# Kernel optimization log

Hardware: AMD Instinct MI355X
Metric: run time of the kernel (lower is better)

Reference implementation:

```python
import jax, jax.numpy as jnp
import numpy as np

EMBED_DIM = 1024
N_HEADS = 16
HEAD_DIM = EMBED_DIM // N_HEADS
SEQ_LEN = 4096


def setup_inputs() -> dict:
    key = jax.random.key(0)
    k1, k2 = jax.random.split(key)
    x = jax.random.normal(k1, (SEQ_LEN, EMBED_DIM), dtype=jnp.float32)
    # Linear params (lecun-normal-ish scale)
    W_qkv = jax.random.normal(k2, (EMBED_DIM, 3 * EMBED_DIM), dtype=jnp.float32) / np.sqrt(EMBED_DIM)
    b_qkv = jnp.zeros((3 * EMBED_DIM,), dtype=jnp.float32)
    return {"x": x, "W_qkv": W_qkv, "b_qkv": b_qkv}


def reference(x, W_qkv, b_qkv):
    T = x.shape[0]
    # Fused QKV projection: [T, 3*E]
    qkv = x @ W_qkv + b_qkv
    q, k, v = jnp.split(qkv, 3, axis=-1)
    # [T, N, H]
    q = q.reshape(T, N_HEADS, HEAD_DIM)
    k = k.reshape(T, N_HEADS, HEAD_DIM)
    v = v.reshape(T, N_HEADS, HEAD_DIM)
    # Standard SDPA (module does NOT pass is_causal, so full attention)
    scale = 1.0 / np.sqrt(HEAD_DIM).astype(np.float32)
    logits = jnp.einsum("qnh,knh->nqk", q, k) * scale  # [N, T, T]
    attn = jax.nn.softmax(logits, axis=-1)
    y = jnp.einsum("nqk,knh->qnh", attn, v)  # [T, N, H]
    return y
```

## Files before the change

kernel.cpp:

```cpp
#include <hip/hip_runtime.h>

#define T_SEQ 4096
#define EMB   1024
#define NH    16
#define HD    64
#define N3    3072

#define SCL2 0.18033688011112042f

using u16 = unsigned short;
using u32 = unsigned int;
typedef __bf16 bf16x8 __attribute__((ext_vector_type(8)));
typedef float  f32x4  __attribute__((ext_vector_type(4)));
typedef float  f32x16 __attribute__((ext_vector_type(16)));
typedef u16    u16x8  __attribute__((ext_vector_type(8)));

#if __has_builtin(__builtin_amdgcn_exp2f)
#define EXP2(x) __builtin_amdgcn_exp2f(x)
#else
#define EXP2(x) exp2f(x)
#endif

__device__ inline u16 f2bf(float f) {
    union { float f; unsigned u; } v; v.f = f;
    unsigned u = v.u;
    u += 0x7FFFu + ((u >> 16) & 1u);
    return (u16)(u >> 16);
}

__global__ void convert_x_kernel(const float* __restrict__ x, u16* __restrict__ xb) {
    int i = (blockIdx.x * 256 + threadIdx.x) * 8;
    float4 a = *(const float4*)(x + i);
    float4 b = *(const float4*)(x + i + 4);
    u16x8 o;
    o[0] = f2bf(a.x); o[1] = f2bf(a.y); o[2] = f2bf(a.z); o[3] = f2bf(a.w);
    o[4] = f2bf(b.x); o[5] = f2bf(b.y); o[6] = f2bf(b.z); o[7] = f2bf(b.w);
    *(u16x8*)(xb + i) = o;
}

__global__ void transpose_w_kernel(const float* __restrict__ W, u16* __restrict__ Wt) {
    __shared__ float tile[64][72];
    int n0 = blockIdx.x * 64, k0 = blockIdx.y * 64;
    float qs = (n0 < 1024) ? SCL2 : 1.0f;
    int t = threadIdx.x;
#pragma unroll
    for (int p = 0; p < 16; ++p) {
        int idx = p * 256 + t;
        int r = idx >> 6, c = idx & 63;
        tile[r][c] = W[(k0 + r) * N3 + n0 + c];
    }
    __syncthreads();
    int c2 = t >> 2;
    int kg = (t & 3) * 16;
    u16x8 o0, o1;
#pragma unroll
    for (int j = 0; j < 8; ++j) o0[j] = f2bf(tile[kg + j][c2] * qs);
#pragma unroll
    for (int j = 0; j < 8; ++j) o1[j] = f2bf(tile[kg + 8 + j][c2] * qs);
    u16* dst = Wt + (n0 + c2) * EMB + k0 + kg;
    *(u16x8*)dst = o0;
    *(u16x8*)(dst + 8) = o1;
}

__global__ __launch_bounds__(256) void gemm_qkv_kernel(const u16* __restrict__ xb,
                                                       const u16* __restrict__ Wt,
                                                       const float* __restrict__ bias,
                                                       u16* __restrict__ qkv) {
    __shared__ __align__(16) u16 Alds[128 * 64];
    __shared__ __align__(16) u16 Blds[128 * 64];
    int tid = threadIdx.x;
    int lane = tid & 63, wave = tid >> 6;
    int wm = wave >> 1, wn = wave & 1;
    int m0 = blockIdx.y * 128, n0 = blockIdx.x * 128;
    int lr = lane & 15, lg = lane >> 4;

    f32x4 acc[4][4] = {};

    for (int kt = 0; kt < 16; ++kt) {
        int kbase = kt * 64;
#pragma unroll
        for (int p = 0; p < 4; ++p) {
            int g = p * 256 + tid;
            int row = g >> 3;
            int cg = (g & 7) << 3;
            int sg = (((cg >> 3) ^ (row & 7)) << 3);
            u16x8 va = *(const u16x8*)(xb + (m0 + row) * EMB + kbase + cg);
            *(u16x8*)&Alds[row * 64 + sg] = va;
            u16x8 vb = *(const u16x8*)(Wt + (n0 + row) * EMB + kbase + cg);
            *(u16x8*)&Blds[row * 64 + sg] = vb;
        }
        __syncthreads();
#pragma unroll
        for (int ks = 0; ks < 2; ++ks) {
            bf16x8 af[4], bf[4];
#pragma unroll
            for (int mi = 0; mi < 4; ++mi) {
                int row = wm * 64 + mi * 16 + lr;
                int sg = ((ks * 4 + lg) ^ (row & 7)) << 3;
                af[mi] = *(const bf16x8*)&Alds[row * 64 + sg];
            }
#pragma unroll
            for (int ni = 0; ni < 4; ++ni) {
                int row = wn * 64 + ni * 16 + lr;
                int sg = ((ks * 4 + lg) ^ (row & 7)) << 3;
                bf[ni] = *(const bf16x8*)&Blds[row * 64 + sg];
            }
#pragma unroll
            for (int mi = 0; mi < 4; ++mi)
#pragma unroll
                for (int ni = 0; ni < 4; ++ni)
                    acc[mi][ni] = __builtin_amdgcn_mfma_f32_16x16x32_bf16(af[mi], bf[ni], acc[mi][ni], 0, 0, 0);
        }
        __syncthreads();
    }
#pragma unroll
    for (int ni = 0; ni < 4; ++ni) {
        int n = n0 + wn * 64 + ni * 16 + lr;
        float bv = bias[n];
        if (n < 1024) bv *= SCL2;
#pragma unroll
        for (int mi = 0; mi < 4; ++mi) {
            int mrow = m0 + wm * 64 + mi * 16 + lg * 4;
#pragma unroll
            for (int r = 0; r < 4; ++r)
                qkv[(mrow + r) * N3 + n] = f2bf(acc[mi][ni][r] + bv);
        }
    }
}

__global__ void transpose_v_kernel(const u16* __restrict__ qkv, u16* __restrict__ Vt) {
    __shared__ u16 tile[64][72];
    int c0 = blockIdx.x * 64;
    int t0 = blockIdx.y * 64;
    int t = threadIdx.x;
#pragma unroll
    for (int p = 0; p < 16; ++p) {
        int idx = p * 256 + t;
        int r = idx >> 6, c = idx & 63;
        tile[r][c] = qkv[(t0 + r) * N3 + 2048 + c0 + c];
    }
    __syncthreads();
    int c2 = t >> 2;
    int kg = (t & 3) * 16;
    u16x8 o0, o1;
#pragma unroll
    for (int j = 0; j < 8; ++j) o0[j] = tile[kg + j][c2];
#pragma unroll
    for (int j = 0; j < 8; ++j) o1[j] = tile[kg + 8 + j][c2];
    u16* dst = Vt + (c0 + c2) * T_SEQ + t0 + kg;
    *(u16x8*)dst = o0;
    *(u16x8*)(dst + 8) = o1;
}

__device__ inline u32 cvtpk(float lo, float hi) {
    u32 r;
    asm("v_cvt_pk_bf16_f32 %0, %1, %2" : "=v"(r) : "v"(lo), "v"(hi));
    return r;
}

__device__ inline bf16x8 mk8(u32 w0, u32 w1, u32 w2, u32 w3) {
    union { u32 w[4]; bf16x8 v; } u;
    u.w[0] = w0; u.w[1] = w1; u.w[2] = w2; u.w[3] = w3;
    return u.v;
}

__device__ inline void pack2(f32x16 p, int hi, bf16x8& fe, bf16x8& fo) {
    u32 a0 = cvtpk(p[0], p[1]),   a1 = cvtpk(p[2], p[3]);
    u32 a2 = cvtpk(p[4], p[5]),   a3 = cvtpk(p[6], p[7]);
    u32 b0 = cvtpk(p[8], p[9]),   b1 = cvtpk(p[10], p[11]);
    u32 b2 = cvtpk(p[12], p[13]), b3 = cvtpk(p[14], p[15]);
    u32 xa0 = (u32)__shfl_xor((int)a0, 32), xa1 = (u32)__shfl_xor((int)a1, 32);
    u32 xa2 = (u32)__shfl_xor((int)a2, 32), xa3 = (u32)__shfl_xor((int)a3, 32);
    u32 xb0 = (u32)__shfl_xor((int)b0, 32), xb1 = (u32)__shfl_xor((int)b1, 32);
    u32 xb2 = (u32)__shfl_xor((int)b2, 32), xb3 = (u32)__shfl_xor((int)b3, 32);
    fe = hi ? mk8(xa2, xa3, a2, a3) : mk8(a0, a1, xa0, xa1);
    fo = hi ? mk8(xb2, xb3, b2, b3) : mk8(b0, b1, xb0, xb1);
}

#define KVROW 72

__global__ __launch_bounds__(256, 2) void attn_kernel(const u16* __restrict__ qkv,
                                                      const u16* __restrict__ Vt,
                                                      float* __restrict__ out) {
    __shared__ __align__(16) char smem[36864];
    u16* K0 = (u16*)smem;
    u16* V0 = (u16*)(smem + 9216);
    u16* K1 = (u16*)(smem + 18432);
    u16* V1 = (u16*)(smem + 27648);

    int tid = threadIdx.x, lane = tid & 63, wave = tid >> 6;
    int ql = lane & 31, hi = lane >> 5;
    int h = blockIdx.y;
    int q0 = blockIdx.x * 128;

    bf16x8 qf[4];
    {
        const u16* qp = qkv + (size_t)(q0 + wave * 32 + ql) * N3 + h * HD;
#pragma unroll
        for (int c = 0; c < 4; ++c)
            qf[c] = *(const bf16x8*)(qp + c * 16 + hi * 8);
    }

    bf16x8 ones;
    {
        union { u16x8 u; bf16x8 b; } uu;
#pragma unroll
        for (int j = 0; j < 8; ++j) uu.u[j] = 0x3F80;
        ones = uu.b;
    }

    f32x16 acc0 = {}, acc1 = {}, acc2 = {};

    int srow0 = tid >> 3, spg = tid & 7;
    int srow1 = srow0 + 32;
    const u16* kptr = qkv + EMB + h * HD;
    const u16* vptr = Vt + (size_t)(h * HD) * T_SEQ;
    int woff0 = srow0 * KVROW + spg * 8;
    int woff1 = srow1 * KVROW + spg * 8;

    u16x8 kst0 = *(const u16x8*)(kptr + (size_t)srow0 * N3 + spg * 8);
    u16x8 kst1 = *(const u16x8*)(kptr + (size_t)srow1 * N3 + spg * 8);
    u16x8 vst0 = *(const u16x8*)(vptr + (size_t)srow0 * T_SEQ + spg * 8);
    u16x8 vst1 = *(const u16x8*)(vptr + (size_t)srow1 * T_SEQ + spg * 8);

    int koff = ql * KVROW + hi * 8;

    for (int t = 0; t < 64; ++t) {
        u16* Kl = (t & 1) ? K1 : K0;
        u16* Vl = (t & 1) ? V1 : V0;
        *(u16x8*)&Kl[woff0] = kst0;
        *(u16x8*)&Kl[woff1] = kst1;
        *(u16x8*)&Vl[woff0] = vst0;
        *(u16x8*)&Vl[woff1] = vst1;
        if (t < 63) {
            const u16* kb = kptr + (size_t)(t + 1) * 64 * N3;
            const u16* vb = vptr + (t + 1) * 64;
            kst0 = *(const u16x8*)(kb + (size_t)srow0 * N3 + spg * 8);
            kst1 = *(const u16x8*)(kb + (size_t)srow1 * N3 + spg * 8);
            vst0 = *(const u16x8*)(vb + (size_t)srow0 * T_SEQ + spg * 8);
            vst1 = *(const u16x8*)(vb + (size_t)srow1 * T_SEQ + spg * 8);
        }
        __syncthreads();

        f32x16 s0 = {}, s1 = {};
#pragma unroll
        for (int c = 0; c < 4; ++c) {
            bf16x8 kf = *(const bf16x8*)&Kl[koff + c * 16];
            s0 = __builtin_amdgcn_mfma_f32_32x32x16_bf16(kf, qf[c], s0, 0, 0, 0);
        }
#pragma unroll
        for (int c = 0; c < 4; ++c) {
            bf16x8 kf = *(const bf16x8*)&Kl[koff + 32 * KVROW + c * 16];
            s1 = __builtin_amdgcn_mfma_f32_32x32x16_bf16(kf, qf[c], s1, 0, 0, 0);
        }

#pragma unroll
        for (int r = 0; r < 16; ++r) s0[r] = EXP2(s0[r]);
#pragma unroll
        for (int r = 0; r < 16; ++r) s1[r] = EXP2(s1[r]);

        bf16x8 pa0, pa1, pa2, pa3;
        pack2(s0, hi, pa0, pa1);
        pack2(s1, hi, pa2, pa3);

#pragma unroll
        for (int c = 0; c < 4; ++c) {
            bf16x8 pb = (c == 0) ? pa0 : (c == 1) ? pa1 : (c == 2) ? pa2 : pa3;
            bf16x8 vf0 = *(const bf16x8*)&Vl[koff + c * 16];
            acc0 = __builtin_amdgcn_mfma_f32_32x32x16_bf16(vf0, pb, acc0, 0, 0, 0);
            bf16x8 vf1 = *(const bf16x8*)&Vl[koff + 32 * KVROW + c * 16];
            acc1 = __builtin_amdgcn_mfma_f32_32x32x16_bf16(vf1, pb, acc1, 0, 0, 0);
            acc2 = __builtin_amdgcn_mfma_f32_32x32x16_bf16(ones, pb, acc2, 0, 0, 0);
        }
    }

    __syncthreads();

    float inv = 1.0f / acc2[0];
    float* ob = (float*)smem + wave * (32 * 68);
#pragma unroll
    for (int g = 0; g < 4; ++g) {
        f32x4 w0 = { acc0[4 * g] * inv, acc0[4 * g + 1] * inv, acc0[4 * g + 2] * inv, acc0[4 * g + 3] * inv };
        *(f32x4*)&ob[ql * 68 + 8 * g + 4 * hi] = w0;
        f32x4 w1 = { acc1[4 * g] * inv, acc1[4 * g + 1] * inv, acc1[4 * g + 2] * inv, acc1[4 * g + 3] * inv };
        *(f32x4*)&ob[ql * 68 + 32 + 8 * g + 4 * hi] = w1;
    }
    asm volatile("s_waitcnt lgkmcnt(0)" ::: "memory");
#pragma unroll
    for (int qq = 0; qq < 8; ++qq) {
        int q = qq * 4 + (lane >> 4);
        int d4 = (lane & 15) * 4;
        f32x4 v = *(const f32x4*)&ob[q * 68 + d4];
        *(f32x4*)&out[(size_t)(q0 + wave * 32 + q) * EMB + h * HD + d4] = v;
    }
}

extern "C" void kernel_launch(void* const* d_in, const int* in_sizes, int n_in,
                              void* d_out, int out_size, void* d_ws, size_t ws_size,
                              hipStream_t stream) {
    (void)in_sizes; (void)n_in; (void)out_size; (void)ws_size;
    const float* x = (const float*)d_in[0];
    const float* W = (const float*)d_in[1];
    const float* b = (const float*)d_in[2];
    float* out = (float*)d_out;

    u16* xb  = (u16*)d_ws;
    u16* Wt  = xb  + (size_t)T_SEQ * EMB;
    u16* qkv = Wt  + (size_t)N3 * EMB;
    u16* Vt  = qkv + (size_t)T_SEQ * N3;

    convert_x_kernel<<<(T_SEQ * EMB) / (256 * 8), 256, 0, stream>>>(x, xb);
    transpose_w_kernel<<<dim3(N3 / 64, EMB / 64), 256, 0, stream>>>(W, Wt);
    gemm_qkv_kernel<<<dim3(N3 / 128, T_SEQ / 128), 256, 0, stream>>>(xb, Wt, b, qkv);
    transpose_v_kernel<<<dim3(EMB / 64, T_SEQ / 64), 256, 0, stream>>>(qkv, Vt);
    attn_kernel<<<dim3(T_SEQ / 128, NH), 256, 0, stream>>>(qkv, Vt, out);
}
```

Before: 150.2 us.

## Split attention KV range across two wave groups and compute row sums on VALU

The attention block grows to 512 threads: two groups of four waves each process half of the key/value sequence for the same 128 queries, then merge their partial outputs and normalisers through shared memory. The softmax denominator is now a VALU sum of the exponentiated scores plus a cross-lane shuffle, replacing the extra MFMA against a ones vector. This aims to double the parallelism per query tile, shorten each wave's serial KV loop and drop a third of the PV-stage MFMAs. In exchange it doubles LDS per block to 72KB, which limits occupancy, and adds a reduction epilogue with extra barriers.

```diff
diff --git a/kernel.cpp b/kernel.cpp
--- a/kernel.cpp
+++ b/kernel.cpp
@@ -164,6 +164,15 @@
     return u.v;
 }
 
+__device__ inline float vsum16(f32x16 v) {
+    float a0 = v[0] + v[1],  a1 = v[2] + v[3];
+    float a2 = v[4] + v[5],  a3 = v[6] + v[7];
+    float a4 = v[8] + v[9],  a5 = v[10] + v[11];
+    float a6 = v[12] + v[13], a7 = v[14] + v[15];
+    float b0 = a0 + a1, b1 = a2 + a3, b2 = a4 + a5, b3 = a6 + a7;
+    return (b0 + b1) + (b2 + b3);
+}
+
 __device__ inline void pack2(f32x16 p, int hi, bf16x8& fe, bf16x8& fo) {
     u32 a0 = cvtpk(p[0], p[1]),   a1 = cvtpk(p[2], p[3]);
     u32 a2 = cvtpk(p[4], p[5]),   a3 = cvtpk(p[6], p[7]);
@@ -179,42 +188,40 @@
 
 #define KVROW 72
 
-__global__ __launch_bounds__(256, 2) void attn_kernel(const u16* __restrict__ qkv,
+__global__ __launch_bounds__(512, 4) void attn_kernel(const u16* __restrict__ qkv,
                                                       const u16* __restrict__ Vt,
                                                       float* __restrict__ out) {
-    __shared__ __align__(16) char smem[36864];
-    u16* K0 = (u16*)smem;
-    u16* V0 = (u16*)(smem + 9216);
-    u16* K1 = (u16*)(smem + 18432);
-    u16* V1 = (u16*)(smem + 27648);
+    __shared__ __align__(16) char smem[73728];
 
     int tid = threadIdx.x, lane = tid & 63, wave = tid >> 6;
     int ql = lane & 31, hi = lane >> 5;
+    int g = tid >> 8;
+    int wq = wave & 3;
+    int tid2 = tid & 255;
     int h = blockIdx.y;
     int q0 = blockIdx.x * 128;
 
+    char* base = smem + g * 36864;
+    u16* K0 = (u16*)base;
+    u16* V0 = (u16*)(base + 9216);
+    u16* K1 = (u16*)(base + 18432);
+    u16* V1 = (u16*)(base + 27648);
+
     bf16x8 qf[4];
     {
-        const u16* qp = qkv + (size_t)(q0 + wave * 32 + ql) * N3 + h * HD;
+        const u16* qp = qkv + (size_t)(q0 + wq * 32 + ql) * N3 + h * HD;
 #pragma unroll
         for (int c = 0; c < 4; ++c)
             qf[c] = *(const bf16x8*)(qp + c * 16 + hi * 8);
     }
 
-    bf16x8 ones;
-    {
-        union { u16x8 u; bf16x8 b; } uu;
-#pragma unroll
-        for (int j = 0; j < 8; ++j) uu.u[j] = 0x3F80;
-        ones = uu.b;
-    }
-
-    f32x16 acc0 = {}, acc1 = {}, acc2 = {};
-
-    int srow0 = tid >> 3, spg = tid & 7;
+    f32x16 acc0 = {}, acc1 = {};
+    float lrun = 0.f;
+
+    int srow0 = tid2 >> 3, spg = tid2 & 7;
     int srow1 = srow0 + 32;
-    const u16* kptr = qkv + EMB + h * HD;
-    const u16* vptr = Vt + (size_t)(h * HD) * T_SEQ;
+    const u16* kptr = qkv + (size_t)(g * 2048) * N3 + EMB + h * HD;
+    const u16* vptr = Vt + (size_t)(h * HD) * T_SEQ + g * 2048;
     int woff0 = srow0 * KVROW + spg * 8;
     int woff1 = srow1 * KVROW + spg * 8;
 
@@ -225,14 +232,14 @@
 
     int koff = ql * KVROW + hi * 8;
 
-    for (int t = 0; t < 64; ++t) {
+    for (int t = 0; t < 32; ++t) {
         u16* Kl = (t & 1) ? K1 : K0;
         u16* Vl = (t & 1) ? V1 : V0;
         *(u16x8*)&Kl[woff0] = kst0;
         *(u16x8*)&Kl[woff1] = kst1;
         *(u16x8*)&Vl[woff0] = vst0;
         *(u16x8*)&Vl[woff1] = vst1;
-        if (t < 63) {
+        if (t < 31) {
             const u16* kb = kptr + (size_t)(t + 1) * 64 * N3;
             const u16* vb = vptr + (t + 1) * 64;
             kst0 = *(const u16x8*)(kb + (size_t)srow0 * N3 + spg * 8);
@@ -259,6 +266,12 @@
 #pragma unroll
         for (int r = 0; r < 16; ++r) s1[r] = EXP2(s1[r]);
 
+        {
+            float ss = vsum16(s0) + vsum16(s1);
+            ss += __shfl_xor(ss, 32);
+            lrun += ss;
+        }
+
         bf16x8 pa0, pa1, pa2, pa3;
         pack2(s0, hi, pa0, pa1);
         pack2(s1, hi, pa2, pa3);
@@ -270,28 +283,54 @@
             acc0 = __builtin_amdgcn_mfma_f32_32x32x16_bf16(vf0, pb, acc0, 0, 0, 0);
             bf16x8 vf1 = *(const bf16x8*)&Vl[koff + 32 * KVROW + c * 16];
             acc1 = __builtin_amdgcn_mfma_f32_32x32x16_bf16(vf1, pb, acc1, 0, 0, 0);
-            acc2 = __builtin_amdgcn_mfma_f32_32x32x16_bf16(ones, pb, acc2, 0, 0, 0);
-        }
-    }
-
-    __syncthreads();
-
-    float inv = 1.0f / acc2[0];
-    float* ob = (float*)smem + wave * (32 * 68);
-#pragma unroll
-    for (int g = 0; g < 4; ++g) {
-        f32x4 w0 = { acc0[4 * g] * inv, acc0[4 * g + 1] * inv, acc0[4 * g + 2] * inv, acc0[4 * g + 3] * inv };
-        *(f32x4*)&ob[ql * 68 + 8 * g + 4 * hi] = w0;
-        f32x4 w1 = { acc1[4 * g] * inv, acc1[4 * g + 1] * inv, acc1[4 * g + 2] * inv, acc1[4 * g + 3] * inv };
-        *(f32x4*)&ob[ql * 68 + 32 + 8 * g + 4 * hi] = w1;
-    }
-    asm volatile("s_waitcnt lgkmcnt(0)" ::: "memory");
-#pragma unroll
-    for (int qq = 0; qq < 8; ++qq) {
-        int q = qq * 4 + (lane >> 4);
-        int d4 = (lane & 15) * 4;
-        f32x4 v = *(const f32x4*)&ob[q * 68 + d4];
-        *(f32x4*)&out[(size_t)(q0 + wave * 32 + q) * EMB + h * HD + d4] = v;
+        }
+    }
+
+    __syncthreads();
+
+    float* Xb = (float*)(smem + 36864);
+    float* lX = Xb + 4 * 32 * 68;
+
+    if (g == 1) {
+        float* ob = Xb + wq * (32 * 68);
+#pragma unroll
+        for (int gg = 0; gg < 4; ++gg) {
+            f32x4 w0 = { acc0[4 * gg], acc0[4 * gg + 1], acc0[4 * gg + 2], acc0[4 * gg + 3] };
+            *(f32x4*)&ob[ql * 68 + 8 * gg + 4 * hi] = w0;
+            f32x4 w1 = { acc1[4 * gg], acc1[4 * gg + 1], acc1[4 * gg + 2], acc1[4 * gg + 3] };
+            *(f32x4*)&ob[ql * 68 + 32 + 8 * gg + 4 * hi] = w1;
+        }
+        if (hi == 0) lX[wq * 32 + ql] = lrun;
+    }
+    __syncthreads();
+
+    if (g == 0) {
+        float* ob = Xb + wq * (32 * 68);
+        float inv = 1.0f / (lrun + lX[wq * 32 + ql]);
+        float* tb = (float*)smem + wq * (32 * 68);
+#pragma unroll
+        for (int gg = 0; gg < 4; ++gg) {
+            f32x4 x0 = *(const f32x4*)&ob[ql * 68 + 8 * gg + 4 * hi];
+            f32x4 w0 = { (acc0[4 * gg] + x0[0]) * inv, (acc0[4 * gg + 1] + x0[1]) * inv,
+                         (acc0[4 * gg + 2] + x0[2]) * inv, (acc0[4 * gg + 3] + x0[3]) * inv };
+            *(f32x4*)&tb[ql * 68 + 8 * gg + 4 * hi] = w0;
+            f32x4 x1 = *(const f32x4*)&ob[ql * 68 + 32 + 8 * gg + 4 * hi];
+            f32x4 w1 = { (acc1[4 * gg] + x1[0]) * inv, (acc1[4 * gg + 1] + x1[1]) * inv,
+                         (acc1[4 * gg + 2] + x1[2]) * inv, (acc1[4 * gg + 3] + x1[3]) * inv };
+            *(f32x4*)&tb[ql * 68 + 32 + 8 * gg + 4 * hi] = w1;
+        }
+    }
+    __syncthreads();
+
+    if (g == 0) {
+        float* tb = (float*)smem + wq * (32 * 68);
+#pragma unroll
+        for (int qq = 0; qq < 8; ++qq) {
+            int q = qq * 4 + (lane >> 4);
+            int d4 = (lane & 15) * 4;
+            f32x4 v = *(const f32x4*)&tb[q * 68 + d4];
+            *(f32x4*)&out[(size_t)(q0 + wq * 32 + q) * EMB + h * HD + d4] = v;
+        }
     }
 }
 
@@ -313,5 +352,5 @@
     transpose_w_kernel<<<dim3(N3 / 64, EMB / 64), 256, 0, stream>>>(W, Wt);
     gemm_qkv_kernel<<<dim3(N3 / 128, T_SEQ / 128), 256, 0, stream>>>(xb, Wt, b, qkv);
     transpose_v_kernel<<<dim3(EMB / 64, T_SEQ / 64), 256, 0, stream>>>(qkv, Vt);
-    attn_kernel<<<dim3(T_SEQ / 128, NH), 256, 0, stream>>>(qkv, Vt, out);
-}
+    attn_kernel<<<dim3(T_SEQ / 128, NH), 512, 0, stream>>>(qkv, Vt, out);
+}
```

Measured after the change: 155.9 us. 3.8% more time.

## Split attention KV range across two blocks and merge partials in combine kernel

Applied to the files above, without the earlier changes.

Attention launches a z-dimension of two, each block processing half of the keys and writing unnormalized partial outputs and row sums; a new combine kernel adds the partials and normalizes. The QKV GEMM now writes separate Q, K, V planes so K loads use a 1024 stride. Partial buffers alias dead workspace regions. This adds an extra kernel and extra global traffic for partials in exchange for more parallel blocks.

```diff
diff --git a/kernel.cpp b/kernel.cpp
--- a/kernel.cpp
+++ b/kernel.cpp
@@ -65,7 +65,7 @@
 __global__ __launch_bounds__(256) void gemm_qkv_kernel(const u16* __restrict__ xb,
                                                        const u16* __restrict__ Wt,
                                                        const float* __restrict__ bias,
-                                                       u16* __restrict__ qkv) {
+                                                       u16* __restrict__ qkv ) {
     __shared__ __align__(16) u16 Alds[128 * 64];
     __shared__ __align__(16) u16 Blds[128 * 64];
     int tid = threadIdx.x;
@@ -118,17 +118,19 @@
         int n = n0 + wn * 64 + ni * 16 + lr;
         float bv = bias[n];
         if (n < 1024) bv *= SCL2;
+        u16* pl = qkv + (size_t)(n >> 10) * ((size_t)T_SEQ * EMB);
+        int nc = n & 1023;
 #pragma unroll
         for (int mi = 0; mi < 4; ++mi) {
             int mrow = m0 + wm * 64 + mi * 16 + lg * 4;
 #pragma unroll
             for (int r = 0; r < 4; ++r)
-                qkv[(mrow + r) * N3 + n] = f2bf(acc[mi][ni][r] + bv);
-        }
-    }
-}
-
-__global__ void transpose_v_kernel(const u16* __restrict__ qkv, u16* __restrict__ Vt) {
+                pl[(size_t)(mrow + r) * EMB + nc] = f2bf(acc[mi][ni][r] + bv);
+        }
+    }
+}
+
+__global__ void transpose_v_kernel(const u16* __restrict__ Vp, u16* __restrict__ Vt) {
     __shared__ u16 tile[64][72];
     int c0 = blockIdx.x * 64;
     int t0 = blockIdx.y * 64;
@@ -137,7 +139,7 @@
     for (int p = 0; p < 16; ++p) {
         int idx = p * 256 + t;
         int r = idx >> 6, c = idx & 63;
-        tile[r][c] = qkv[(t0 + r) * N3 + 2048 + c0 + c];
+        tile[r][c] = Vp[(size_t)(t0 + r) * EMB + c0 + c];
     }
     __syncthreads();
     int c2 = t >> 2;
@@ -179,9 +181,14 @@
 
 #define KVROW 72
 
-__global__ __launch_bounds__(256, 2) void attn_kernel(const u16* __restrict__ qkv,
+__global__ __launch_bounds__(256, 2) void attn_kernel(const u16* __restrict__ Qp,
+                                                      const u16* __restrict__ Kp,
                                                       const u16* __restrict__ Vt,
-                                                      float* __restrict__ out) {
+                                                      float* __restrict__ out,
+                                                      float* __restrict__ pA,
+                                                      float* __restrict__ pB,
+                                                      float* __restrict__ l0,
+                                                      float* __restrict__ l1) {
     __shared__ __align__(16) char smem[36864];
     u16* K0 = (u16*)smem;
     u16* V0 = (u16*)(smem + 9216);
@@ -192,10 +199,11 @@
     int ql = lane & 31, hi = lane >> 5;
     int h = blockIdx.y;
     int q0 = blockIdx.x * 128;
+    int half = blockIdx.z;
 
     bf16x8 qf[4];
     {
-        const u16* qp = qkv + (size_t)(q0 + wave * 32 + ql) * N3 + h * HD;
+        const u16* qp = Qp + (size_t)(q0 + wave * 32 + ql) * EMB + h * HD;
 #pragma unroll
         for (int c = 0; c < 4; ++c)
             qf[c] = *(const bf16x8*)(qp + c * 16 + hi * 8);
@@ -213,30 +221,30 @@
 
     int srow0 = tid >> 3, spg = tid & 7;
     int srow1 = srow0 + 32;
-    const u16* kptr = qkv + EMB + h * HD;
-    const u16* vptr = Vt + (size_t)(h * HD) * T_SEQ;
+    const u16* kptr = Kp + (size_t)(half * 2048) * EMB + h * HD;
+    const u16* vptr = Vt + (size_t)(h * HD) * T_SEQ + half * 2048;
     int woff0 = srow0 * KVROW + spg * 8;
     int woff1 = srow1 * KVROW + spg * 8;
 
-    u16x8 kst0 = *(const u16x8*)(kptr + (size_t)srow0 * N3 + spg * 8);
-    u16x8 kst1 = *(const u16x8*)(kptr + (size_t)srow1 * N3 + spg * 8);
+    u16x8 kst0 = *(const u16x8*)(kptr + (size_t)srow0 * EMB + spg * 8);
+    u16x8 kst1 = *(const u16x8*)(kptr + (size_t)srow1 * EMB + spg * 8);
     u16x8 vst0 = *(const u16x8*)(vptr + (size_t)srow0 * T_SEQ + spg * 8);
     u16x8 vst1 = *(const u16x8*)(vptr + (size_t)srow1 * T_SEQ + spg * 8);
 
     int koff = ql * KVROW + hi * 8;
 
-    for (int t = 0; t < 64; ++t) {
+    for (int t = 0; t < 32; ++t) {
         u16* Kl = (t & 1) ? K1 : K0;
         u16* Vl = (t & 1) ? V1 : V0;
         *(u16x8*)&Kl[woff0] = kst0;
         *(u16x8*)&Kl[woff1] = kst1;
         *(u16x8*)&Vl[woff0] = vst0;
         *(u16x8*)&Vl[woff1] = vst1;
-        if (t < 63) {
-            const u16* kb = kptr + (size_t)(t + 1) * 64 * N3;
+        if (t < 31) {
+            const u16* kb = kptr + (size_t)(t + 1) * 64 * EMB;
             const u16* vb = vptr + (t + 1) * 64;
-            kst0 = *(const u16x8*)(kb + (size_t)srow0 * N3 + spg * 8);
-            kst1 = *(const u16x8*)(kb + (size_t)srow1 * N3 + spg * 8);
+            kst0 = *(const u16x8*)(kb + (size_t)srow0 * EMB + spg * 8);
+            kst1 = *(const u16x8*)(kb + (size_t)srow1 * EMB + spg * 8);
             vst0 = *(const u16x8*)(vb + (size_t)srow0 * T_SEQ + spg * 8);
             vst1 = *(const u16x8*)(vb + (size_t)srow1 * T_SEQ + spg * 8);
         }
@@ -276,23 +284,58 @@
 
     __syncthreads();
 
-    float inv = 1.0f / acc2[0];
+    if (hi == 0) {
+        float* dl = half ? l1 : l0;
+        dl[h * T_SEQ + q0 + wave * 32 + ql] = acc2[0];
+    }
+
     float* ob = (float*)smem + wave * (32 * 68);
 #pragma unroll
     for (int g = 0; g < 4; ++g) {
-        f32x4 w0 = { acc0[4 * g] * inv, acc0[4 * g + 1] * inv, acc0[4 * g + 2] * inv, acc0[4 * g + 3] * inv };
+        f32x4 w0 = { acc0[4 * g], acc0[4 * g + 1], acc0[4 * g + 2], acc0[4 * g + 3] };
         *(f32x4*)&ob[ql * 68 + 8 * g + 4 * hi] = w0;
-        f32x4 w1 = { acc1[4 * g] * inv, acc1[4 * g + 1] * inv, acc1[4 * g + 2] * inv, acc1[4 * g + 3] * inv };
+        f32x4 w1 = { acc1[4 * g], acc1[4 * g + 1], acc1[4 * g + 2], acc1[4 * g + 3] };
         *(f32x4*)&ob[ql * 68 + 32 + 8 * g + 4 * hi] = w1;
     }
     asm volatile("s_waitcnt lgkmcnt(0)" ::: "memory");
-#pragma unroll
-    for (int qq = 0; qq < 8; ++qq) {
-        int q = qq * 4 + (lane >> 4);
-        int d4 = (lane & 15) * 4;
-        f32x4 v = *(const f32x4*)&ob[q * 68 + d4];
-        *(f32x4*)&out[(size_t)(q0 + wave * 32 + q) * EMB + h * HD + d4] = v;
-    }
+    if (half == 0) {
+#pragma unroll
+        for (int qq = 0; qq < 8; ++qq) {
+            int q = qq * 4 + (lane >> 4);
+            int d4 = (lane & 15) * 4;
+            f32x4 v = *(const f32x4*)&ob[q * 68 + d4];
+            *(f32x4*)&out[(size_t)(q0 + wave * 32 + q) * EMB + h * HD + d4] = v;
+        }
+    } else {
+        float* P1h = (h < 14) ? (pA + (size_t)h * (T_SEQ * HD))
+                              : (pB + (size_t)(h - 14) * (T_SEQ * HD));
+#pragma unroll
+        for (int qq = 0; qq < 8; ++qq) {
+            int q = qq * 4 + (lane >> 4);
+            int d4 = (lane & 15) * 4;
+            f32x4 v = *(const f32x4*)&ob[q * 68 + d4];
+            *(f32x4*)&P1h[(size_t)(q0 + wave * 32 + q) * HD + d4] = v;
+        }
+    }
+}
+
+__global__ void combine_kernel(float* __restrict__ out,
+                               const float* __restrict__ pA,
+                               const float* __restrict__ pB,
+                               const float* __restrict__ l0,
+                               const float* __restrict__ l1) {
+    size_t idx = ((size_t)blockIdx.x * 256 + threadIdx.x) * 4;
+    int q = (int)(idx >> 10);
+    int e = (int)(idx & 1023);
+    int h = e >> 6, d = e & 63;
+    const float* p1 = (h < 14) ? (pA + (size_t)h * (T_SEQ * HD))
+                               : (pB + (size_t)(h - 14) * (T_SEQ * HD));
+    f32x4 o = *(const f32x4*)&out[idx];
+    f32x4 p = *(const f32x4*)&p1[(size_t)q * HD + d];
+    float inv = 1.0f / (l0[h * T_SEQ + q] + l1[h * T_SEQ + q]);
+    f32x4 r = { (o[0] + p[0]) * inv, (o[1] + p[1]) * inv,
+                (o[2] + p[2]) * inv, (o[3] + p[3]) * inv };
+    *(f32x4*)&out[idx] = r;
 }
 
 extern "C" void kernel_launch(void* const* d_in, const int* in_sizes, int n_in,
@@ -304,14 +347,21 @@
     const float* b = (const float*)d_in[2];
     float* out = (float*)d_out;
 
-    u16* xb  = (u16*)d_ws;
-    u16* Wt  = xb  + (size_t)T_SEQ * EMB;
-    u16* qkv = Wt  + (size_t)N3 * EMB;
-    u16* Vt  = qkv + (size_t)T_SEQ * N3;
+    u16* xb = (u16*)d_ws;
+    u16* Wt = xb + (size_t)T_SEQ * EMB;
+    u16* Qp = Wt + (size_t)N3 * EMB;
+    u16* Kp = Qp + (size_t)T_SEQ * EMB;
+    u16* Vp = Kp + (size_t)T_SEQ * EMB;
+    u16* Vt = Vp + (size_t)T_SEQ * EMB;
+    float* pA = (float*)d_ws;
+    float* pB = (float*)Vp;
+    float* l0 = pB + 2 * (size_t)T_SEQ * HD;
+    float* l1 = l0 + (size_t)NH * T_SEQ;
 
     convert_x_kernel<<<(T_SEQ * EMB) / (256 * 8), 256, 0, stream>>>(x, xb);
     transpose_w_kernel<<<dim3(N3 / 64, EMB / 64), 256, 0, stream>>>(W, Wt);
-    gemm_qkv_kernel<<<dim3(N3 / 128, T_SEQ / 128), 256, 0, stream>>>(xb, Wt, b, qkv);
-    transpose_v_kernel<<<dim3(EMB / 64, T_SEQ / 64), 256, 0, stream>>>(qkv, Vt);
-    attn_kernel<<<dim3(T_SEQ / 128, NH), 256, 0, stream>>>(qkv, Vt, out);
-}
+    gemm_qkv_kernel<<<dim3(N3 / 128, T_SEQ / 128), 256, 0, stream>>>(xb, Wt, b, Qp);
+    transpose_v_kernel<<<dim3(EMB / 64, T_SEQ / 64), 256, 0, stream>>>(Vp, Vt);
+    attn_kernel<<<dim3(T_SEQ / 128, NH, 2), 256, 0, stream>>>(Qp, Kp, Vt, out, pA, pB, l0, l1);
+    combine_kernel<<<(T_SEQ * EMB) / (256 * 4), 256, 0, stream>>>(out, pA, pB, l0, l1);
+}
```

Result: slower. 160.9 us (+7.1%).
